# Kernel optimization log

Hardware: AMD Instinct MI355X
Metric: run time of the kernel (lower is better)

Reference implementation:

```python
import jax, jax.numpy as jnp
import numpy as np

B, S, D = 2, 2048, 2048
NH, NG = 16, 4          # q heads, groups
KVH = NH // NG          # kv heads = 4
HD = D // NH            # head dim = 128
ROPE_THETA = 10000.0


def _rope(t, cos, sin):
    """Rotate pairs along last dim. t: [B,S,D]; cos/sin: [S, D//2]."""
    tr = t.reshape(t.shape[:-1] + (-1, 2))  # [B,S,D/2,2] complex pairs (llama layout)
    xr, xi = tr[..., 0], tr[..., 1]
    c = cos[None, :, :]
    s = sin[None, :, :]
    yr = xr * c - xi * s
    yi = xr * s + xi * c
    return jnp.stack([yr, yi], axis=-1).reshape(t.shape)


def setup_inputs() -> dict:
    key = jax.random.key(0)
    k0, k1, k2, k3, k4 = jax.random.split(key, 5)
    scale = 1.0 / np.sqrt(D)
    x = jax.random.normal(k0, (B, S, D), jnp.float32)
    Wq = jax.random.normal(k1, (D, D), jnp.float32) * scale          # torch Linear: (out,in)
    Wk = jax.random.normal(k2, (D // NG, D), jnp.float32) * scale
    Wv = jax.random.normal(k3, (D // NG, D), jnp.float32) * scale
    Wo = jax.random.normal(k4, (D, D), jnp.float32) * scale
    mask = jnp.triu(jnp.ones((S, S), bool), k=1)[None, None]          # causal: True = masked
    return {"x": x, "Wq": Wq, "Wk": Wk, "Wv": Wv, "Wo": Wo, "mask": mask}


def reference(x, Wq, Wk, Wv, Wo, mask):
    b, s, d = x.shape
    q = x @ Wq.T                                  # [B,S,D]
    k = x @ Wk.T                                  # [B,S,D/NG]
    v = x @ Wv.T
    # repeat_kv: [B,S,KVH,HD] -> repeat each kv head NG times -> [B,S,NH,HD]
    k = jnp.repeat(k.reshape(b, s, KVH, HD), NG, axis=2).reshape(b, s, d)
    v = jnp.repeat(v.reshape(b, s, KVH, HD), NG, axis=2).reshape(b, s, d)
    # RoPE with freqs precomputed over the FULL hidden dim (as in source)
    freqs = 1.0 / (ROPE_THETA ** (jnp.arange(0, d, 2, dtype=jnp.float32) / d))  # [D/2]
    ang = jnp.arange(s, dtype=jnp.float32)[:, None] * freqs[None, :]            # [S,D/2]
    cos, sin = jnp.cos(ang), jnp.sin(ang)
    q = _rope(q, cos, sin)
    k = _rope(k, cos, sin)
    # split heads: [B,NH,S,HD]
    qh = q.reshape(b, s, NH, HD).transpose(0, 2, 1, 3)
    kh = k.reshape(b, s, NH, HD).transpose(0, 2, 1, 3)
    vh = v.reshape(b, s, NH, HD).transpose(0, 2, 1, 3)
    # NOTE: source scales by sqrt(hidden_dim), not sqrt(head_dim)
    scores = jnp.einsum('bhqd,bhkd->bhqk', qh, kh) / jnp.sqrt(jnp.float32(d))
    scores = jnp.where(mask, -jnp.inf, scores)
    probs = jax.nn.softmax(scores, axis=-1)
    out = jnp.einsum('bhqk,bhkd->bhqd', probs, vh)
    out = out.transpose(0, 2, 1, 3).reshape(b, s, d)
    return out @ Wo.T  # dropout is identity in eval
```

## Files before the change

kernel.cpp:

```cpp
#include <hip/hip_runtime.h>
#include <hip/hip_bf16.h>
#include <stdint.h>

typedef unsigned short u16;
typedef u16 u16x4 __attribute__((ext_vector_type(4)));
typedef unsigned u32x4 __attribute__((ext_vector_type(4)));
typedef __bf16 bf16x8 __attribute__((ext_vector_type(8)));
typedef float f32x4 __attribute__((ext_vector_type(4)));
typedef float f32x16 __attribute__((ext_vector_type(16)));

#define DEVI __device__ __forceinline__

DEVI u16 f2b(float f) {
  __hip_bfloat16 h = __float2bfloat16(f);
  return __builtin_bit_cast(u16, h);
}

DEVI unsigned pk2(float lo, float hi) {
  return (unsigned)f2b(lo) | ((unsigned)f2b(hi) << 16);
}

DEVI f32x4 mfma16(bf16x8 a, bf16x8 b, f32x4 c) {
  return __builtin_amdgcn_mfma_f32_16x16x32_bf16(a, b, c, 0, 0, 0);
}

DEVI f32x16 mfma32(bf16x8 a, bf16x8 b, f32x16 c) {
  return __builtin_amdgcn_mfma_f32_32x32x16_bf16(a, b, c, 0, 0, 0);
}

DEVI void gld_lds16(const u16* g, u16* l) {
  __builtin_amdgcn_global_load_lds(
      (const __attribute__((address_space(1))) unsigned int*)g,
      (__attribute__((address_space(3))) unsigned int*)l, 16, 0, 0);
}

__global__ void cvt_all(const float4* __restrict__ x, const float4* __restrict__ wq,
                        const float4* __restrict__ wk, const float4* __restrict__ wv,
                        const float4* __restrict__ wo,
                        u16x4* __restrict__ xb, u16x4* __restrict__ wqb,
                        u16x4* __restrict__ wkb, u16x4* __restrict__ wvb,
                        u16x4* __restrict__ wob) {
  long i = (long)blockIdx.x * 256 + threadIdx.x;
  const float4* src; u16x4* dst; long o;
  if (i < 2097152)      { src = x;  dst = xb;  o = i; }
  else if (i < 3145728) { src = wq; dst = wqb; o = i - 2097152; }
  else if (i < 3407872) { src = wk; dst = wkb; o = i - 3145728; }
  else if (i < 3670016) { src = wv; dst = wvb; o = i - 3407872; }
  else                  { src = wo; dst = wob; o = i - 3670016; }
  float4 v = src[o];
  u16x4 r = { f2b(v.x), f2b(v.y), f2b(v.z), f2b(v.w) };
  dst[o] = r;
}

__global__ void rope_table(float2* __restrict__ csT) {
  int i = blockIdx.x * 256 + threadIdx.x;
  int s = i >> 10, p = i & 1023;
  float freq = exp2f((float)p * -0.012976281620653759f);
  float ang = (float)s * freq;
  float sv, cv;
  __sincosf(ang, &sv, &cv);
  csT[i] = make_float2(cv, sv);
}

__global__ __launch_bounds__(256)
void gemm_qkv(const u16* __restrict__ A, const u16* __restrict__ wq,
              const u16* __restrict__ wk, const u16* __restrict__ wv,
              const float2* __restrict__ csT, u16* __restrict__ Qh,
              u16* __restrict__ Kh, u16* __restrict__ Vtp) {
  __shared__ __align__(16) u16 lds[2][2][4096];
  const int tid = threadIdx.x;
  const int lane = tid & 63;
  const int w = tid >> 6;
  const int wr = w >> 1, wc = w & 1;
  const int x = blockIdx.x, m0 = blockIdx.y << 7, n0 = x << 7;
  const int K = 2048;

  const u16* Bw;
  int mode;
  if (x < 16)      { Bw = wq + (size_t)n0 * K;          mode = 0; }
  else if (x < 20) { Bw = wk + (size_t)(n0 - 2048) * K; mode = 1; }
  else             { Bw = wv + (size_t)(n0 - 2560) * K; mode = 2; }

  const int srow = tid >> 2;
  const int schunk = (tid & 3) << 3;
  const int p4 = srow >> 4, pl = srow & 15;
  const int prow = (pl << 1) | (p4 & 1) | ((p4 & 2) << 4);
  const int bsrc = (mode == 2) ? srow : prow;
  const u16* ga0 = A + (size_t)(m0 + srow) * K + schunk;
  const u16* gb0 = Bw + (size_t)bsrc * K + schunk;
  const size_t rstep = (size_t)64 * K;

  f32x4 acc[4][4] = {};
  const int nk = K >> 5;
  int cur = 0;

  {
    u16* la = &lds[0][0][tid << 3];
    u16* lb = &lds[0][1][tid << 3];
    gld_lds16(ga0, la);
    gld_lds16(ga0 + rstep, la + 2048);
    gld_lds16(gb0, lb);
    gld_lds16(gb0 + rstep, lb + 2048);
  }
  __syncthreads();

  const int l15 = lane & 15;
  const int kcol = (lane >> 4) << 3;
  const int arow = ((wr << 6) + l15) << 5;
  const int brow = ((wc << 6) + l15) << 5;

  for (int kt = 0; kt < nk; ++kt) {
    if (kt + 1 < nk) {
      const u16* ga = ga0 + ((size_t)(kt + 1) << 5);
      const u16* gb = gb0 + ((size_t)(kt + 1) << 5);
      u16* la = &lds[cur ^ 1][0][tid << 3];
      u16* lb = &lds[cur ^ 1][1][tid << 3];
      gld_lds16(ga, la);
      gld_lds16(ga + rstep, la + 2048);
      gld_lds16(gb, lb);
      gld_lds16(gb + rstep, lb + 2048);
    }
    const u16* la = &lds[cur][0][0];
    const u16* lb = &lds[cur][1][0];
    bf16x8 af[4], bfr[4];
#pragma unroll
    for (int mi = 0; mi < 4; ++mi)
      af[mi] = *(const bf16x8*)&la[arow + (mi << 9) + kcol];
#pragma unroll
    for (int ni = 0; ni < 4; ++ni)
      bfr[ni] = *(const bf16x8*)&lb[brow + (ni << 9) + kcol];
#pragma unroll
    for (int mi = 0; mi < 4; ++mi)
#pragma unroll
      for (int ni = 0; ni < 4; ++ni)
        acc[mi][ni] = mfma16(af[mi], bfr[ni], acc[mi][ni]);
    __syncthreads();
    cur ^= 1;
  }

  const int crow = (lane >> 4) << 2;
  if (mode == 0) {
    const float SCL = 0.022097086912079608f * 1.4426950408889634f;
    const int h = x;
    const int qb = (wc << 6) + (l15 << 1);
    const int tb = (n0 >> 1) + (wc << 5) + l15;
#pragma unroll
    for (int mi = 0; mi < 4; ++mi)
#pragma unroll
      for (int rr = 0; rr < 4; ++rr) {
        int row = m0 + (wr << 6) + (mi << 4) + crow + rr;
        int s = row & 2047, b = row >> 11;
        float2 cA = csT[(s << 10) + tb];
        float2 cB = csT[(s << 10) + tb + 16];
        float v0 = acc[mi][0][rr], v1 = acc[mi][1][rr];
        float v2 = acc[mi][2][rr], v3 = acc[mi][3][rr];
        unsigned lo = pk2((v0 * cA.x - v1 * cA.y) * SCL, (v0 * cA.y + v1 * cA.x) * SCL);
        unsigned hi = pk2((v2 * cB.x - v3 * cB.y) * SCL, (v2 * cB.y + v3 * cB.x) * SCL);
        u16* dst = &Qh[((size_t)(b * 16 + h) * 2048 + s) * 128 + qb];
        *(unsigned*)dst = lo;
        *(unsigned*)(dst + 32) = hi;
      }
  } else if (mode == 1) {
    const int kvh = x - 16;
    const int qb = (wc << 6) + (l15 << 1);
#pragma unroll
    for (int mi = 0; mi < 4; ++mi)
#pragma unroll
      for (int rr = 0; rr < 4; ++rr) {
        int row = m0 + (wr << 6) + (mi << 4) + crow + rr;
        int s = row & 2047, b = row >> 11;
        float v0 = acc[mi][0][rr], v1 = acc[mi][1][rr];
        float v2 = acc[mi][2][rr], v3 = acc[mi][3][rr];
#pragma unroll
        for (int g = 0; g < 4; ++g) {
          int h = (kvh << 2) + g;
          int tb = (h << 6) + (wc << 5) + l15;
          float2 cA = csT[(s << 10) + tb];
          float2 cB = csT[(s << 10) + tb + 16];
          unsigned lo = pk2(v0 * cA.x - v1 * cA.y, v0 * cA.y + v1 * cA.x);
          unsigned hi = pk2(v2 * cB.x - v3 * cB.y, v2 * cB.y + v3 * cB.x);
          u16* dst = &Kh[((size_t)(b * 16 + h) * 2048 + s) * 128 + qb];
          *(unsigned*)dst = lo;
          *(unsigned*)(dst + 32) = hi;
        }
      }
  } else {
    const int ccol = l15;
#pragma unroll
    for (int mi = 0; mi < 4; ++mi) {
      int sg = m0 + (wr << 6) + (mi << 4) + crow;
      int b = sg >> 11, s = sg & 2047;
#pragma unroll
      for (int ni = 0; ni < 4; ++ni) {
        int n = (n0 - 2560) + (wc << 6) + (ni << 4) + ccol;
        u16x4 pk = { f2b(acc[mi][ni][0]), f2b(acc[mi][ni][1]),
                     f2b(acc[mi][ni][2]), f2b(acc[mi][ni][3]) };
        *(u16x4*)&Vtp[((size_t)((b << 2) + (n >> 7)) * 128 + (n & 127)) * 2048 + s] = pk;
      }
    }
  }
}

__global__ __launch_bounds__(256)
void gemm_bt(const u16* __restrict__ A, const u16* __restrict__ Bw,
             float* __restrict__ C, int M, int N, int K) {
  __shared__ __align__(16) u16 lds[2][2][4096];
  const int tid = threadIdx.x;
  const int lane = tid & 63;
  const int w = tid >> 6;
  const int wr = w >> 1, wc = w & 1;
  const int m0 = blockIdx.y << 7, n0 = blockIdx.x << 7;

  const int srow = tid >> 2;
  const int schunk = (tid & 3) << 3;
  const u16* ga0 = A + (size_t)(m0 + srow) * K + schunk;
  const u16* gb0 = Bw + (size_t)(n0 + srow) * K + schunk;
  const size_t rstep = (size_t)64 * K;

  f32x4 acc[4][4] = {};
  const int nk = K >> 5;
  int cur = 0;

  {
    u16* la = &lds[0][0][tid << 3];
    u16* lb = &lds[0][1][tid << 3];
    gld_lds16(ga0, la);
    gld_lds16(ga0 + rstep, la + 2048);
    gld_lds16(gb0, lb);
    gld_lds16(gb0 + rstep, lb + 2048);
  }
  __syncthreads();

  const int l15 = lane & 15;
  const int kcol = (lane >> 4) << 3;
  const int arow = ((wr << 6) + l15) << 5;
  const int brow = ((wc << 6) + l15) << 5;

  for (int kt = 0; kt < nk; ++kt) {
    if (kt + 1 < nk) {
      const u16* ga = ga0 + ((size_t)(kt + 1) << 5);
      const u16* gb = gb0 + ((size_t)(kt + 1) << 5);
      u16* la = &lds[cur ^ 1][0][tid << 3];
      u16* lb = &lds[cur ^ 1][1][tid << 3];
      gld_lds16(ga, la);
      gld_lds16(ga + rstep, la + 2048);
      gld_lds16(gb, lb);
      gld_lds16(gb + rstep, lb + 2048);
    }
    const u16* la = &lds[cur][0][0];
    const u16* lb = &lds[cur][1][0];
    bf16x8 af[4], bfr[4];
#pragma unroll
    for (int mi = 0; mi < 4; ++mi)
      af[mi] = *(const bf16x8*)&la[arow + (mi << 9) + kcol];
#pragma unroll
    for (int ni = 0; ni < 4; ++ni)
      bfr[ni] = *(const bf16x8*)&lb[brow + (ni << 9) + kcol];
#pragma unroll
    for (int mi = 0; mi < 4; ++mi)
#pragma unroll
      for (int ni = 0; ni < 4; ++ni)
        acc[mi][ni] = mfma16(af[mi], bfr[ni], acc[mi][ni]);
    __syncthreads();
    cur ^= 1;
  }

  const int crow = (lane >> 4) << 2;
  const int ccol = lane & 15;
#pragma unroll
  for (int mi = 0; mi < 4; ++mi) {
    int row = m0 + (wr << 6) + (mi << 4) + crow;
#pragma unroll
    for (int ni = 0; ni < 4; ++ni) {
      int col = n0 + (wc << 6) + (ni << 4) + ccol;
#pragma unroll
      for (int rr = 0; rr < 4; ++rr)
        C[(size_t)(row + rr) * N + col] = acc[mi][ni][rr];
    }
  }
}

__global__ __launch_bounds__(256, 2)
void attn_kernel(const u16* __restrict__ Qh, const u16* __restrict__ Kh,
                 const u16* __restrict__ Vt, u16* __restrict__ attnO) {
  __shared__ __align__(16) u16 lds[3][8192];
  const int tid = threadIdx.x, lane = tid & 63, w = tid >> 6;
  const int bid = blockIdx.x;
  const int x = bid & 7, j = bid >> 3;
  const int half = j >> 5, jj = j & 31;
  const int bh = (x << 2) + (jj >> 4) + (half << 1);
  const int r = jj & 15;
  const int qt = half ? r : 15 - r;
  const int h = bh & 15, b = bh >> 4;

  const int qi = lane & 31, hi = lane >> 5;
  const int q0 = (qt << 7) + (w << 5);
  const int qabs = q0 + qi;

  const u16* Qp = Qh + (size_t)(b * 16 + h) * 262144;
  const u16* Kp = Kh + (size_t)(b * 16 + h) * 262144;
  const u16* Vp = Vt + (size_t)((b << 2) + (h >> 2)) * 262144;

  bf16x8 qf[8];
#pragma unroll
  for (int kc = 0; kc < 8; ++kc)
    qf[kc] = *(const bf16x8*)&Qp[(size_t)qabs * 128 + kc * 16 + hi * 8];

  const int kRow = tid >> 4;
  const int kCl = ((tid & 15) ^ (kRow & 7)) << 3;
  const int vRow = tid >> 2;
  const int vCl = ((tid & 3) ^ ((tid >> 3) & 3)) << 3;
  const int ldsoff = tid << 3;

  f32x16 ot[4] = {};
  float mrow = -1e30f, lsum = 0.f;
  const int nt = (qt << 2) + 4;
  const int nt_w = (qt << 2) + w + 1;
  const int swq = qi & 7, swv = (qi >> 1) & 3;

#pragma unroll
  for (int pt = 0; pt < 2; ++pt) {
    u16* bb = (u16*)lds[pt];
    gld_lds16(Kp + (size_t)((pt << 5) + kRow) * 128 + kCl, bb + ldsoff);
    gld_lds16(Kp + (size_t)((pt << 5) + kRow + 16) * 128 + kCl, bb + ldsoff + 2048);
    gld_lds16(Vp + (size_t)vRow * 2048 + (pt << 5) + vCl, bb + 4096 + ldsoff);
    gld_lds16(Vp + (size_t)(vRow + 64) * 2048 + (pt << 5) + vCl, bb + 4096 + ldsoff + 2048);
  }

  int bufc = 0;
  for (int t = 0; t < nt; ++t) {
    asm volatile("s_waitcnt vmcnt(4)" ::: "memory");
    __builtin_amdgcn_sched_barrier(0);
    __builtin_amdgcn_s_barrier();
    {
      const int ts = (t + 2 < nt) ? t + 2 : nt - 1;
      const int bufn = bufc ? bufc - 1 : 2;
      u16* bb = (u16*)lds[bufn];
      gld_lds16(Kp + (size_t)((ts << 5) + kRow) * 128 + kCl, bb + ldsoff);
      gld_lds16(Kp + (size_t)((ts << 5) + kRow + 16) * 128 + kCl, bb + ldsoff + 2048);
      gld_lds16(Vp + (size_t)vRow * 2048 + (ts << 5) + vCl, bb + 4096 + ldsoff);
      gld_lds16(Vp + (size_t)(vRow + 64) * 2048 + (ts << 5) + vCl, bb + 4096 + ldsoff + 2048);
    }
    if (t < nt_w) {
      const u16* kb_ = &lds[bufc][0];
      const u16* vb_ = &lds[bufc][4096];
      f32x16 st = {};
      __builtin_amdgcn_s_setprio(1);
#pragma unroll
      for (int kc = 0; kc < 8; ++kc) {
        bf16x8 kf = *(const bf16x8*)&kb_[(qi << 7) + ((((kc << 1) + hi) ^ swq) << 3)];
        st = mfma32(kf, qf[kc], st);
      }
      __builtin_amdgcn_s_setprio(0);

      if (t == nt_w - 1) {
        const int kb0 = t << 5;
#pragma unroll
        for (int reg = 0; reg < 16; ++reg) {
          int kk = kb0 + (reg & 3) + ((reg >> 2) << 3) + (hi << 2);
          if (kk > qabs) st[reg] = -1e30f;
        }
      }

      float tmax = st[0];
#pragma unroll
      for (int reg = 1; reg < 16; ++reg) tmax = fmaxf(tmax, st[reg]);
      tmax = fmaxf(tmax, __shfl_xor(tmax, 32));

      if (__any(tmax - mrow > 11.5f)) {
        float nm = fmaxf(mrow, tmax);
        float al = __builtin_amdgcn_exp2f(mrow - nm);
        mrow = nm;
        lsum *= al;
#pragma unroll
        for (int db = 0; db < 4; ++db)
#pragma unroll
          for (int reg = 0; reg < 16; ++reg) ot[db][reg] *= al;
      }

      float psum = 0.f;
#pragma unroll
      for (int reg = 0; reg < 16; ++reg) {
        st[reg] = __builtin_amdgcn_exp2f(st[reg] - mrow);
        psum += st[reg];
      }
      psum += __shfl_xor(psum, 32);
      lsum += psum;

      bf16x8 pfrag[2];
#pragma unroll
      for (int bbp = 0; bbp < 2; ++bbp) {
        unsigned x0 = pk2(st[8 * bbp + 0], st[8 * bbp + 1]);
        unsigned x1 = pk2(st[8 * bbp + 2], st[8 * bbp + 3]);
        unsigned y0 = pk2(st[8 * bbp + 4], st[8 * bbp + 5]);
        unsigned y1 = pk2(st[8 * bbp + 6], st[8 * bbp + 7]);
        asm("v_permlane32_swap_b32 %0, %1" : "+v"(x0), "+v"(y0));
        asm("v_permlane32_swap_b32 %0, %1" : "+v"(x1), "+v"(y1));
        u32x4 uw = { x0, x1, y0, y1 };
        pfrag[bbp] = __builtin_bit_cast(bf16x8, uw);
      }

      __builtin_amdgcn_s_setprio(1);
#pragma unroll
      for (int db = 0; db < 4; ++db) {
        const u16* vr = &vb_[((db << 5) + qi) << 5];
#pragma unroll
        for (int ks = 0; ks < 2; ++ks) {
          bf16x8 vf = *(const bf16x8*)&vr[((((ks << 1) + hi)) ^ swv) << 3];
          ot[db] = mfma32(vf, pfrag[ks], ot[db]);
        }
      }
      __builtin_amdgcn_s_setprio(0);
    }
    bufc = (bufc == 2) ? 0 : bufc + 1;
  }

  float inv = 1.f / lsum;
  u16* rowp = attnO + (size_t)(b * 2048 + qabs) * 2048 + h * 128 + (hi << 2);
#pragma unroll
  for (int db = 0; db < 4; ++db)
#pragma unroll
    for (int mg = 0; mg < 4; ++mg) {
      u16x4 pkv = { f2b(ot[db][4 * mg + 0] * inv), f2b(ot[db][4 * mg + 1] * inv),
                    f2b(ot[db][4 * mg + 2] * inv), f2b(ot[db][4 * mg + 3] * inv) };
      *(u16x4*)&rowp[(db << 5) + (mg << 3)] = pkv;
    }
}

extern "C" void kernel_launch(void* const* d_in, const int* in_sizes, int n_in,
                              void* d_out, int out_size, void* d_ws, size_t ws_size,
                              hipStream_t stream) {
  const float* x  = (const float*)d_in[0];
  const float* Wq = (const float*)d_in[1];
  const float* Wk = (const float*)d_in[2];
  const float* Wv = (const float*)d_in[3];
  const float* Wo = (const float*)d_in[4];
  float* out = (float*)d_out;
  char* ws = (char*)d_ws;

  u16*    xb   = (u16*)(ws + 0);
  u16*    wqb  = (u16*)(ws + 16777216);
  u16*    wkb  = (u16*)(ws + 25165824);
  u16*    wvb  = (u16*)(ws + 27262976);
  u16*    wob  = (u16*)(ws + 29360128);
  float2* csT  = (float2*)(ws + 37748736);
  u16*    Qhp  = (u16*)(ws + 54525952);
  u16*    Khp  = (u16*)(ws + 71303168);
  u16*    Vtp  = (u16*)(ws + 88080384);
  u16*    attnb= (u16*)(ws + 92274688);

  cvt_all<<<18432, 256, 0, stream>>>((const float4*)x, (const float4*)Wq,
                                     (const float4*)Wk, (const float4*)Wv,
                                     (const float4*)Wo, (u16x4*)xb, (u16x4*)wqb,
                                     (u16x4*)wkb, (u16x4*)wvb, (u16x4*)wob);
  rope_table<<<8192, 256, 0, stream>>>(csT);
  gemm_qkv<<<dim3(24, 32), 256, 0, stream>>>(xb, wqb, wkb, wvb, csT, Qhp, Khp, Vtp);
  attn_kernel<<<512, 256, 0, stream>>>(Qhp, Khp, Vtp, attnb);
  gemm_bt<<<dim3(16, 32), 256, 0, stream>>>(attnb, wob, out, 4096, 2048, 2048);
}
```

Baseline: 219.6 us.

## Swizzle GEMM LDS chunks, fuse prep kernels, raise occupancy hint

XOR-swizzles the 16-byte K-chunk position per row pair in the LDS tiles of both GEMMs, so MFMA fragment reads from LDS hit distinct banks instead of conflicting. The bf16 conversion and RoPE table kernels are merged into one launch to save a kernel launch. Launch bounds now request 5 waves-per-EU occupancy, which caps registers per thread and may cause spills.

```diff
diff --git a/kernel.cpp b/kernel.cpp
--- a/kernel.cpp
+++ b/kernel.cpp
@@ -34,13 +34,24 @@
       (__attribute__((address_space(3))) unsigned int*)l, 16, 0, 0);
 }
 
-__global__ void cvt_all(const float4* __restrict__ x, const float4* __restrict__ wq,
-                        const float4* __restrict__ wk, const float4* __restrict__ wv,
-                        const float4* __restrict__ wo,
-                        u16x4* __restrict__ xb, u16x4* __restrict__ wqb,
-                        u16x4* __restrict__ wkb, u16x4* __restrict__ wvb,
-                        u16x4* __restrict__ wob) {
-  long i = (long)blockIdx.x * 256 + threadIdx.x;
+__global__ void prep(const float4* __restrict__ x, const float4* __restrict__ wq,
+                     const float4* __restrict__ wk, const float4* __restrict__ wv,
+                     const float4* __restrict__ wo,
+                     u16x4* __restrict__ xb, u16x4* __restrict__ wqb,
+                     u16x4* __restrict__ wkb, u16x4* __restrict__ wvb,
+                     u16x4* __restrict__ wob, float2* __restrict__ csT) {
+  long bid = blockIdx.x;
+  if (bid < 8192) {
+    int i = (int)bid * 256 + threadIdx.x;
+    int s = i >> 10, p = i & 1023;
+    float freq = exp2f((float)p * -0.012976281620653759f);
+    float ang = (float)s * freq;
+    float sv, cv;
+    __sincosf(ang, &sv, &cv);
+    csT[i] = make_float2(cv, sv);
+    return;
+  }
+  long i = (bid - 8192) * 256 + threadIdx.x;
   const float4* src; u16x4* dst; long o;
   if (i < 2097152)      { src = x;  dst = xb;  o = i; }
   else if (i < 3145728) { src = wq; dst = wqb; o = i - 2097152; }
@@ -52,17 +63,7 @@
   dst[o] = r;
 }
 
-__global__ void rope_table(float2* __restrict__ csT) {
-  int i = blockIdx.x * 256 + threadIdx.x;
-  int s = i >> 10, p = i & 1023;
-  float freq = exp2f((float)p * -0.012976281620653759f);
-  float ang = (float)s * freq;
-  float sv, cv;
-  __sincosf(ang, &sv, &cv);
-  csT[i] = make_float2(cv, sv);
-}
-
-__global__ __launch_bounds__(256)
+__global__ __launch_bounds__(256, 5)
 void gemm_qkv(const u16* __restrict__ A, const u16* __restrict__ wq,
               const u16* __restrict__ wk, const u16* __restrict__ wv,
               const float2* __restrict__ csT, u16* __restrict__ Qh,
@@ -82,12 +83,12 @@
   else             { Bw = wv + (size_t)(n0 - 2560) * K; mode = 2; }
 
   const int srow = tid >> 2;
-  const int schunk = (tid & 3) << 3;
+  const int cs = (tid & 3) ^ ((srow >> 1) & 3);
   const int p4 = srow >> 4, pl = srow & 15;
   const int prow = (pl << 1) | (p4 & 1) | ((p4 & 2) << 4);
   const int bsrc = (mode == 2) ? srow : prow;
-  const u16* ga0 = A + (size_t)(m0 + srow) * K + schunk;
-  const u16* gb0 = Bw + (size_t)bsrc * K + schunk;
+  const u16* ga0 = A + (size_t)(m0 + srow) * K + (cs << 3);
+  const u16* gb0 = Bw + (size_t)bsrc * K + (cs << 3);
   const size_t rstep = (size_t)64 * K;
 
   f32x4 acc[4][4] = {};
@@ -105,9 +106,10 @@
   __syncthreads();
 
   const int l15 = lane & 15;
-  const int kcol = (lane >> 4) << 3;
-  const int arow = ((wr << 6) + l15) << 5;
-  const int brow = ((wc << 6) + l15) << 5;
+  const int lg = lane >> 4;
+  const int ch8 = (lg ^ ((l15 >> 1) & 3)) << 3;
+  const int abase = (((wr << 6) + l15) << 5) + ch8;
+  const int bbase = (((wc << 6) + l15) << 5) + ch8;
 
   for (int kt = 0; kt < nk; ++kt) {
     if (kt + 1 < nk) {
@@ -125,10 +127,10 @@
     bf16x8 af[4], bfr[4];
 #pragma unroll
     for (int mi = 0; mi < 4; ++mi)
-      af[mi] = *(const bf16x8*)&la[arow + (mi << 9) + kcol];
+      af[mi] = *(const bf16x8*)&la[abase + (mi << 9)];
 #pragma unroll
     for (int ni = 0; ni < 4; ++ni)
-      bfr[ni] = *(const bf16x8*)&lb[brow + (ni << 9) + kcol];
+      bfr[ni] = *(const bf16x8*)&lb[bbase + (ni << 9)];
 #pragma unroll
     for (int mi = 0; mi < 4; ++mi)
 #pragma unroll
@@ -201,7 +203,7 @@
   }
 }
 
-__global__ __launch_bounds__(256)
+__global__ __launch_bounds__(256, 5)
 void gemm_bt(const u16* __restrict__ A, const u16* __restrict__ Bw,
              float* __restrict__ C, int M, int N, int K) {
   __shared__ __align__(16) u16 lds[2][2][4096];
@@ -212,9 +214,9 @@
   const int m0 = blockIdx.y << 7, n0 = blockIdx.x << 7;
 
   const int srow = tid >> 2;
-  const int schunk = (tid & 3) << 3;
-  const u16* ga0 = A + (size_t)(m0 + srow) * K + schunk;
-  const u16* gb0 = Bw + (size_t)(n0 + srow) * K + schunk;
+  const int cs = (tid & 3) ^ ((srow >> 1) & 3);
+  const u16* ga0 = A + (size_t)(m0 + srow) * K + (cs << 3);
+  const u16* gb0 = Bw + (size_t)(n0 + srow) * K + (cs << 3);
   const size_t rstep = (size_t)64 * K;
 
   f32x4 acc[4][4] = {};
@@ -232,9 +234,10 @@
   __syncthreads();
 
   const int l15 = lane & 15;
-  const int kcol = (lane >> 4) << 3;
-  const int arow = ((wr << 6) + l15) << 5;
-  const int brow = ((wc << 6) + l15) << 5;
+  const int lg = lane >> 4;
+  const int ch8 = (lg ^ ((l15 >> 1) & 3)) << 3;
+  const int abase = (((wr << 6) + l15) << 5) + ch8;
+  const int bbase = (((wc << 6) + l15) << 5) + ch8;
 
   for (int kt = 0; kt < nk; ++kt) {
     if (kt + 1 < nk) {
@@ -252,10 +255,10 @@
     bf16x8 af[4], bfr[4];
 #pragma unroll
     for (int mi = 0; mi < 4; ++mi)
-      af[mi] = *(const bf16x8*)&la[arow + (mi << 9) + kcol];
+      af[mi] = *(const bf16x8*)&la[abase + (mi << 9)];
 #pragma unroll
     for (int ni = 0; ni < 4; ++ni)
-      bfr[ni] = *(const bf16x8*)&lb[brow + (ni << 9) + kcol];
+      bfr[ni] = *(const bf16x8*)&lb[bbase + (ni << 9)];
 #pragma unroll
     for (int mi = 0; mi < 4; ++mi)
 #pragma unroll
@@ -449,11 +452,10 @@
   u16*    Vtp  = (u16*)(ws + 88080384);
   u16*    attnb= (u16*)(ws + 92274688);
 
-  cvt_all<<<18432, 256, 0, stream>>>((const float4*)x, (const float4*)Wq,
-                                     (const float4*)Wk, (const float4*)Wv,
-                                     (const float4*)Wo, (u16x4*)xb, (u16x4*)wqb,
-                                     (u16x4*)wkb, (u16x4*)wvb, (u16x4*)wob);
-  rope_table<<<8192, 256, 0, stream>>>(csT);
+  prep<<<26624, 256, 0, stream>>>((const float4*)x, (const float4*)Wq,
+                                  (const float4*)Wk, (const float4*)Wv,
+                                  (const float4*)Wo, (u16x4*)xb, (u16x4*)wqb,
+                                  (u16x4*)wkb, (u16x4*)wvb, (u16x4*)wob, csT);
   gemm_qkv<<<dim3(24, 32), 256, 0, stream>>>(xb, wqb, wkb, wvb, csT, Qhp, Khp, Vtp);
   attn_kernel<<<512, 256, 0, stream>>>(Qhp, Khp, Vtp, attnb);
   gemm_bt<<<dim3(16, 32), 256, 0, stream>>>(attnb, wob, out, 4096, 2048, 2048);
```

New measurement: 298.3 us. 1.36x slower.
